# Optimization experiments

Hardware: AMD Instinct MI355X
Metric: run time of the kernel (lower is better)

The kernel has to match this reference:

```python
import jax, jax.numpy as jnp
import numpy as np

B, H0, C_IN, C_OUT, K = 8, 32, 512, 512, 3
H1 = 2 * H0  # 64, resolution after bilinear upsample


def _mod_conv(x, conv_w, s):
    """StyleGAN2 modulate+demodulate per-sample conv.
    x: [B,H,W,Cin]; conv_w: [k,k,Cin,Cout]; s: [B,Cout] style scales.
    Implemented as one grouped conv (groups=B) instead of a Python loop.
    """
    wp = conv_w[None] * s[:, None, None, None, :]              # [B,k,k,Cin,Cout]
    d = jax.lax.rsqrt(jnp.sum(wp * wp, axis=(1, 2, 3)) + 1e-8)  # [B,Cout] demod
    wp = wp * d[:, None, None, None, :]
    Bn, H, W, Ci = x.shape
    Co = wp.shape[-1]
    xg = jnp.transpose(x, (1, 2, 0, 3)).reshape(1, H, W, Bn * Ci)
    kg = jnp.transpose(wp, (1, 2, 3, 0, 4)).reshape(wp.shape[1], wp.shape[2], Ci, Bn * Co)
    out = jax.lax.conv_general_dilated(
        xg, kg, (1, 1), 'SAME',
        dimension_numbers=('NHWC', 'HWIO', 'NHWC'),
        feature_group_count=Bn)
    return jnp.transpose(out.reshape(H, W, Bn, Co), (2, 0, 1, 3))


def setup_inputs() -> dict:
    key = jax.random.key(0)
    ks = jax.random.split(key, 13)
    g = 0.02
    return {
        'x': jax.random.uniform(ks[0], (B, H0, H0, C_IN), jnp.float32),
        'w': jax.random.uniform(ks[1], (B, 512), jnp.float32),
        'noise': jax.random.uniform(ks[2], (1, 1, 1, C_OUT), jnp.float32),
        'y0_kernel': jax.random.normal(ks[3], (512, C_OUT), jnp.float32) * g,
        'y0_bias': jnp.zeros((C_OUT,), jnp.float32),
        'y1_kernel': jax.random.normal(ks[4], (512, C_OUT), jnp.float32) * g,
        'y1_bias': jnp.zeros((C_OUT,), jnp.float32),
        'conv0': jax.random.normal(ks[5], (K, K, C_IN, C_OUT), jnp.float32) * g,
        'conv1': jax.random.normal(ks[6], (K, K, C_OUT, C_OUT), jnp.float32) * g,
        'noise_scale0': jax.random.normal(ks[7], (B, H1, H1, C_OUT), jnp.float32) * g,
        'noise_scale1': jax.random.normal(ks[8], (B, H1, H1, C_OUT), jnp.float32) * g,
        'bias0': jax.random.normal(ks[9], (B, H1, H1, C_OUT), jnp.float32) * g,
        'bias1': jax.random.normal(ks[10], (B, H1, H1, C_OUT), jnp.float32) * g,
    }


def reference(x, w, noise, y0_kernel, y0_bias, y1_kernel, y1_bias,
              conv0, conv1, noise_scale0, noise_scale1, bias0, bias1):
    x = jax.image.resize(x, (x.shape[0], 2 * x.shape[1], 2 * x.shape[2], x.shape[3]),
                         method='bilinear')
    s0 = w @ y0_kernel + y0_bias                 # Dense y_0
    x = _mod_conv(x, conv0, s0)
    x = x + noise_scale0 * noise + bias0
    x = jax.nn.leaky_relu(x, 0.2)
    # NOTE: the original TF code computes the second modulated conv but never
    # assigns its result back to x (the tf.concat is missing). We replicate
    # that math faithfully: the conv output is computed and discarded.
    s1 = w @ y1_kernel + y1_bias
    _unused = _mod_conv(x, conv1, s1)
    x = x + noise_scale1 * noise + bias1
    return jax.nn.leaky_relu(x, 0.2)
```

## Files before the change

### kernel.cpp

```cpp
#include <hip/hip_runtime.h>
#include <stdint.h>

typedef __attribute__((ext_vector_type(8))) __bf16 bf16x8;
typedef __attribute__((ext_vector_type(4))) float f32x4;
typedef __attribute__((ext_vector_type(2))) float f32x2;
typedef __attribute__((ext_vector_type(8))) unsigned short us8;

__device__ __forceinline__ unsigned short f2bf(float f) {
  unsigned u = __float_as_uint(f);
  unsigned r = u + 0x7fffu + ((u >> 16) & 1u);
  return (unsigned short)(r >> 16);
}

__device__ __forceinline__ void gload16(const void* gptr, void* lptr) {
  __builtin_amdgcn_global_load_lds(
      (const __attribute__((address_space(1))) void*)gptr,
      (__attribute__((address_space(3))) void*)lptr, 16, 0, 0);
}

__global__ void k_bpack(const float* __restrict__ conv0,
                        unsigned short* __restrict__ bpack,
                        float* __restrict__ wpart) {
  __shared__ float tile[64][65];
  int bx = blockIdx.x;
  int tap = bx >> 6, rem = bx & 63;
  int chunk = rem >> 3, cb = rem & 7;
  int ci0 = chunk << 6, co0 = cb << 6;
  int ty = threadIdx.x >> 6, tx = threadIdx.x & 63;
#pragma unroll
  for (int k = 0; k < 16; ++k) {
    int ci = (k << 2) + ty;
    tile[ci][tx] = conv0[((size_t)(tap * 512 + ci0 + ci)) * 512 + co0 + tx];
  }
  __syncthreads();
  float p = 0.f;
#pragma unroll
  for (int q = 0; q < 16; ++q) {
    float v = tile[(ty << 4) + q][tx];
    p += v * v;
  }
  __shared__ float red[4][64];
  red[ty][tx] = p;
  __syncthreads();
  if (ty == 0)
    wpart[(size_t)(chunk * 9 + tap) * 512 + co0 + tx] =
        red[0][tx] + red[1][tx] + red[2][tx] + red[3][tx];
#pragma unroll
  for (int s2 = 0; s2 < 2; ++s2) {
    int slot = (threadIdx.x << 1) + s2;
    int f = slot >> 6, l = slot & 63;
    int co16l = f >> 1, kk = f & 1;
    int col = (co16l << 4) + (l & 15);
    int cil = (kk << 5) + ((l >> 4) << 3);
    us8 o;
#pragma unroll
    for (int e = 0; e < 8; ++e) o[e] = f2bf(tile[cil + e][col]);
    size_t fi = (((size_t)chunk * 9 + tap) * 32 + (cb << 2) + co16l) * 2 + kk;
    *(us8*)(bpack + fi * 512 + (size_t)l * 8) = o;
  }
}

__global__ void k_scale(const float* __restrict__ w, const float* __restrict__ y0k,
                        const float* __restrict__ y0b, const float* __restrict__ wpart,
                        float* __restrict__ scale) {
  int g = blockIdx.x * 256 + threadIdx.x;
  int b = g >> 9, co = g & 511;
  float s = y0b[co];
  const float* wr = w + b * 512;
  for (int ci = 0; ci < 512; ++ci) s += wr[ci] * y0k[ci * 512 + co];
  float ws = 0.f;
  for (int r = 0; r < 72; ++r) ws += wpart[(size_t)r * 512 + co];
  scale[g] = s * rsqrtf(s * s * ws + 1e-8f);
}

__global__ void k_up(const float* __restrict__ x, unsigned short* __restrict__ xpad) {
  int gid = blockIdx.x * 256 + threadIdx.x;
  if (gid >= 8 * 66 * 66 * 64) return;
  int c0 = (gid & 63) << 3;
  int pos = gid >> 6;
  int xx = pos % 66;
  int t = pos / 66;
  int yy = t % 66;
  int b = t / 66;
  unsigned short* dst = xpad + (size_t)pos * 512 + c0;
  us8 o;
  if (yy == 0 || yy == 65 || xx == 0 || xx == 65) {
#pragma unroll
    for (int i = 0; i < 8; ++i) o[i] = 0;
  } else {
    int y = yy - 1, xq = xx - 1;
    int jy = y >> 1, jx = xq >> 1;
    int r0, r1, cx0, cx1;
    float ay0, ay1, ax0, ax1;
    if ((y & 1) == 0) { r0 = jy > 0 ? jy - 1 : 0; r1 = jy;
      ay0 = jy > 0 ? 0.25f : 0.f; ay1 = jy > 0 ? 0.75f : 1.f;
    } else { r0 = jy; r1 = jy < 31 ? jy + 1 : 31;
      ay0 = jy < 31 ? 0.75f : 1.f; ay1 = jy < 31 ? 0.25f : 0.f; }
    if ((xq & 1) == 0) { cx0 = jx > 0 ? jx - 1 : 0; cx1 = jx;
      ax0 = jx > 0 ? 0.25f : 0.f; ax1 = jx > 0 ? 0.75f : 1.f;
    } else { cx0 = jx; cx1 = jx < 31 ? jx + 1 : 31;
      ax0 = jx < 31 ? 0.75f : 1.f; ax1 = jx < 31 ? 0.25f : 0.f; }
    const float* base = x + (size_t)b * 32 * 32 * 512 + c0;
    const f32x4* q00 = (const f32x4*)(base + (size_t)(r0 * 32 + cx0) * 512);
    const f32x4* q01 = (const f32x4*)(base + (size_t)(r0 * 32 + cx1) * 512);
    const f32x4* q10 = (const f32x4*)(base + (size_t)(r1 * 32 + cx0) * 512);
    const f32x4* q11 = (const f32x4*)(base + (size_t)(r1 * 32 + cx1) * 512);
#pragma unroll
    for (int h = 0; h < 2; ++h) {
      f32x4 a = q00[h], bb = q01[h], c = q10[h], d = q11[h];
#pragma unroll
      for (int e = 0; e < 4; ++e) {
        float v = ay0 * (ax0 * a[e] + ax1 * bb[e]) + ay1 * (ax0 * c[e] + ax1 * d[e]);
        o[h * 4 + e] = f2bf(v);
      }
    }
  }
  *(us8*)dst = o;
}

__global__ __launch_bounds__(256) void k_conv(
    const unsigned short* __restrict__ xpad,
    const unsigned short* __restrict__ bpack,
    const float* __restrict__ scale,
    const float* __restrict__ noise,
    const float* __restrict__ ns0, const float* __restrict__ ns1,
    const float* __restrict__ bias0, const float* __restrict__ bias1,
    float* __restrict__ out)
{
  __shared__ __align__(16) unsigned short ldsA[2][16896];

  const int tid = threadIdx.x;
  const int wid = tid >> 6;
  const int lane = tid & 63;
  const int l15 = lane & 15, lhi = lane >> 4;

  const int bx = blockIdx.x;
  const int nblk = (bx >> 1) & 3;
  const int mblk = ((bx >> 3) << 1) | (bx & 1);
  const int b = mblk >> 5;
  const int y0 = (mblk & 31) << 1;
  const int wr = wid >> 1, wc = wid & 1;
  const int co_base = (nblk << 7) + (wc << 6);

  f32x4 acc[4][4];
#pragma unroll
  for (int i = 0; i < 4; ++i)
#pragma unroll
    for (int j = 0; j < 4; ++j) acc[i][j] = f32x4{0.f, 0.f, 0.f, 0.f};

  const size_t xb = (size_t)b * (66 * 66 * 512);
  const size_t wboff = (size_t)((nblk << 3) + (wc << 2)) * 1024 + (size_t)lane * 8;
  bf16x8 bq0[8], bq1[8];

  {
#pragma unroll
    for (int i = wid; i < 33; i += 4) {
      int g = (i << 6) + lane;
      int rx = g >> 3;
      int r = rx / 66;
      int xx = rx - r * 66;
      int cg = (g & 7) ^ (xx & 7);
      const unsigned short* src =
          xpad + xb + ((size_t)((y0 + r) * 66 + xx) << 9) + (cg << 3);
      gload16(src, (char*)ldsA[0] + (i << 10));
    }
    const unsigned short* wb = bpack + wboff;
#pragma unroll
    for (int ni = 0; ni < 4; ++ni)
#pragma unroll
      for (int kk = 0; kk < 2; ++kk)
        bq0[ni * 2 + kk] = *(const bf16x8*)(wb + ni * 1024 + kk * 512);
  }
  __syncthreads();

  for (int chunk = 0; chunk < 8; ++chunk) {
    const char* Acur = (const char*)ldsA[chunk & 1];
    const unsigned short* wb = bpack + (size_t)chunk * 294912 + wboff;

#pragma unroll
    for (int tap = 0; tap < 9; ++tap) {
      auto& cur = (tap & 1) ? bq1 : bq0;
      auto& nxt = (tap & 1) ? bq0 : bq1;
      if (tap < 8) {
#pragma unroll
        for (int ni = 0; ni < 4; ++ni)
#pragma unroll
          for (int kk = 0; kk < 2; ++kk)
            nxt[ni * 2 + kk] =
                *(const bf16x8*)(wb + (tap + 1) * 32768 + ni * 1024 + kk * 512);
      } else if (chunk < 7) {
#pragma unroll
        for (int ni = 0; ni < 4; ++ni)
#pragma unroll
          for (int kk = 0; kk < 2; ++kk)
            nxt[ni * 2 + kk] =
                *(const bf16x8*)(wb + 294912 + ni * 1024 + kk * 512);
      }
      if (tap == 0 && chunk < 7) {
        char* Anxt = (char*)ldsA[(chunk + 1) & 1];
        const int kc = (chunk + 1) << 6;
#pragma unroll
        for (int i = wid; i < 33; i += 4) {
          int g = (i << 6) + lane;
          int rx = g >> 3;
          int r = rx / 66;
          int xx = rx - r * 66;
          int cg = (g & 7) ^ (xx & 7);
          const unsigned short* src =
              xpad + xb + ((size_t)((y0 + r) * 66 + xx) << 9) + kc + (cg << 3);
          gload16(src, Anxt + (i << 10));
        }
      }
      const int ky = tap / 3, kx = tap - ky * 3;
      const int r = wr + ky;
      const int axor = ((l15 + kx) & 7) << 4;
#pragma unroll
      for (int kk = 0; kk < 2; ++kk) {
        const int kbyte = (((kk << 5) + (lhi << 3)) << 1);
        bf16x8 af[4];
#pragma unroll
        for (int mi = 0; mi < 4; ++mi) {
          int xx = (mi << 4) + l15 + kx;
          int off = ((r * 66 + xx) << 7) + (kbyte ^ axor);
          af[mi] = *(const bf16x8*)(Acur + off);
        }
        __builtin_amdgcn_s_setprio(1);
#pragma unroll
        for (int mi = 0; mi < 4; ++mi)
#pragma unroll
          for (int ni = 0; ni < 4; ++ni)
            acc[mi][ni] = __builtin_amdgcn_mfma_f32_16x16x32_bf16(
                af[mi], cur[ni * 2 + kk], acc[mi][ni], 0, 0, 0);
        __builtin_amdgcn_s_setprio(0);
      }
    }
#pragma unroll
    for (int i = 0; i < 8; ++i) bq0[i] = bq1[i];
    __syncthreads();
  }

  float* ldsE = (float*)ldsA + wid * 4224;
  float sc[4];
#pragma unroll
  for (int ni = 0; ni < 4; ++ni)
    sc[ni] = scale[(b << 9) + co_base + (ni << 4) + l15];
#pragma unroll
  for (int mi = 0; mi < 4; ++mi)
#pragma unroll
    for (int ni = 0; ni < 4; ++ni)
#pragma unroll
      for (int j = 0; j < 4; ++j) {
        int px = (mi << 4) + (lhi << 2) + j;
        ldsE[px * 66 + (ni << 4) + l15] = acc[mi][ni][j] * sc[ni];
      }
  const int qd = l15;
  const int py = y0 + wr;
  const f32x4 nz4 = *(const f32x4*)(noise + co_base + (qd << 2));
#pragma unroll
  for (int q = 0; q < 16; ++q) {
    int px = (q << 2) + lhi;
    f32x2 v01 = *(const f32x2*)(ldsE + px * 66 + (qd << 2));
    f32x2 v23 = *(const f32x2*)(ldsE + px * 66 + (qd << 2) + 2);
    size_t idx = (((size_t)((b << 6) + py) << 6) + px) * 512 + co_base + (qd << 2);
    f32x4 a0 = *(const f32x4*)(ns0 + idx);
    f32x4 b0 = *(const f32x4*)(bias0 + idx);
    f32x4 a1 = *(const f32x4*)(ns1 + idx);
    f32x4 b1 = *(const f32x4*)(bias1 + idx);
    f32x4 o;
    float vv[4] = {v01[0], v01[1], v23[0], v23[1]};
#pragma unroll
    for (int e = 0; e < 4; ++e) {
      float v0 = vv[e] + a0[e] * nz4[e] + b0[e];
      v0 = fmaxf(v0, 0.2f * v0);
      v0 = v0 + a1[e] * nz4[e] + b1[e];
      o[e] = fmaxf(v0, 0.2f * v0);
    }
    *(f32x4*)(out + idx) = o;
  }
}

extern "C" void kernel_launch(void* const* d_in, const int* in_sizes, int n_in,
                              void* d_out, int out_size, void* d_ws, size_t ws_size,
                              hipStream_t stream) {
  const float* x     = (const float*)d_in[0];
  const float* w     = (const float*)d_in[1];
  const float* noise = (const float*)d_in[2];
  const float* y0k   = (const float*)d_in[3];
  const float* y0b   = (const float*)d_in[4];
  const float* conv0 = (const float*)d_in[7];
  const float* ns0   = (const float*)d_in[9];
  const float* ns1   = (const float*)d_in[10];
  const float* bias0 = (const float*)d_in[11];
  const float* bias1 = (const float*)d_in[12];
  float* out = (float*)d_out;

  char* ws = (char*)d_ws;
  unsigned short* xpad  = (unsigned short*)ws;
  unsigned short* bpack = (unsigned short*)(ws + 35684352);
  float* scale = (float*)(ws + 35684352 + 4718592);
  float* wpart = (float*)(ws + 35684352 + 4718592 + 16384);

  k_bpack<<<576, 256, 0, stream>>>(conv0, bpack, wpart);
  k_scale<<<16, 256, 0, stream>>>(w, y0k, y0b, wpart, scale);
  k_up<<<8712, 256, 0, stream>>>(x, xpad);
  k_conv<<<1024, 256, 0, stream>>>(xpad, bpack, scale, noise, ns0, ns1, bias0, bias1, out);
}
```

Baseline: 215.4 us.

## Deepen conv weight prefetch to two taps and double-buffer LDS A fragments

The main conv loop now keeps three register buffers for the weight fragments, loaded two taps ahead. A flat tap index runs across chunk boundaries, so the loop no longer needs a copy between buffers. The activation fragments for the next tap are read from LDS into a second register set while the current tap's MFMAs run, which is meant to hide both global and LDS load latency behind matrix math. The launch bounds now request two blocks per CU. The extra live registers could cause spills or lower occupancy.

```diff
diff --git a/kernel.cpp b/kernel.cpp
--- a/kernel.cpp
+++ b/kernel.cpp
@@ -55,7 +55,7 @@
     us8 o;
 #pragma unroll
     for (int e = 0; e < 8; ++e) o[e] = f2bf(tile[cil + e][col]);
-    size_t fi = (((size_t)chunk * 9 + tap) * 32 + (cb << 2) + co16l) * 2 + kk;
+    size_t fi = (((size_t)(chunk * 9 + tap) * 32 + (cb << 2) + co16l) << 1) + kk;
     *(us8*)(bpack + fi * 512 + (size_t)l * 8) = o;
   }
 }
@@ -118,7 +118,7 @@
   *(us8*)dst = o;
 }
 
-__global__ __launch_bounds__(256) void k_conv(
+__global__ __launch_bounds__(256, 2) void k_conv(
     const unsigned short* __restrict__ xpad,
     const unsigned short* __restrict__ bpack,
     const float* __restrict__ scale,
@@ -149,8 +149,39 @@
     for (int j = 0; j < 4; ++j) acc[i][j] = f32x4{0.f, 0.f, 0.f, 0.f};
 
   const size_t xb = (size_t)b * (66 * 66 * 512);
-  const size_t wboff = (size_t)((nblk << 3) + (wc << 2)) * 1024 + (size_t)lane * 8;
-  bf16x8 bq0[8], bq1[8];
+  const unsigned short* wbase =
+      bpack + ((size_t)((nblk << 3) + (wc << 2)) << 10) + (size_t)lane * 8;
+
+  bf16x8 afA[8], afB[8];
+  bf16x8 bqA[8], bqB[8], bqC[8];
+
+#define LOAD_BQ(DST, T)                                                        \
+  {                                                                            \
+    const unsigned short* wp = wbase + (size_t)(T) * 32768;                    \
+    _Pragma("unroll")                                                          \
+    for (int ni = 0; ni < 4; ++ni) {                                           \
+      _Pragma("unroll")                                                        \
+      for (int kk = 0; kk < 2; ++kk)                                           \
+        (DST)[ni * 2 + kk] = *(const bf16x8*)(wp + ni * 1024 + kk * 512);      \
+    }                                                                          \
+  }
+
+#define LOAD_AF(DST, TAP)                                                      \
+  {                                                                            \
+    const int ky_ = (TAP) / 3, kx_ = (TAP) - ky_ * 3;                          \
+    const int r_ = wr + ky_;                                                   \
+    const int axor_ = ((l15 + kx_) & 7) << 4;                                  \
+    _Pragma("unroll")                                                          \
+    for (int kk = 0; kk < 2; ++kk) {                                           \
+      const int kbyte_ = (((kk << 5) + (lhi << 3)) << 1);                      \
+      _Pragma("unroll")                                                        \
+      for (int mi = 0; mi < 4; ++mi) {                                         \
+        int xx_ = (mi << 4) + l15 + kx_;                                       \
+        int off_ = ((r_ * 66 + xx_) << 7) + (kbyte_ ^ axor_);                  \
+        (DST)[kk * 4 + mi] = *(const bf16x8*)(Acur + off_);                    \
+      }                                                                        \
+    }                                                                          \
+  }
 
   {
 #pragma unroll
@@ -164,39 +195,25 @@
           xpad + xb + ((size_t)((y0 + r) * 66 + xx) << 9) + (cg << 3);
       gload16(src, (char*)ldsA[0] + (i << 10));
     }
-    const unsigned short* wb = bpack + wboff;
-#pragma unroll
-    for (int ni = 0; ni < 4; ++ni)
-#pragma unroll
-      for (int kk = 0; kk < 2; ++kk)
-        bq0[ni * 2 + kk] = *(const bf16x8*)(wb + ni * 1024 + kk * 512);
+    LOAD_BQ(bqA, 0)
+    LOAD_BQ(bqB, 1)
   }
   __syncthreads();
 
   for (int chunk = 0; chunk < 8; ++chunk) {
     const char* Acur = (const char*)ldsA[chunk & 1];
-    const unsigned short* wb = bpack + (size_t)chunk * 294912 + wboff;
-
-#pragma unroll
-    for (int tap = 0; tap < 9; ++tap) {
-      auto& cur = (tap & 1) ? bq1 : bq0;
-      auto& nxt = (tap & 1) ? bq0 : bq1;
-      if (tap < 8) {
-#pragma unroll
-        for (int ni = 0; ni < 4; ++ni)
-#pragma unroll
-          for (int kk = 0; kk < 2; ++kk)
-            nxt[ni * 2 + kk] =
-                *(const bf16x8*)(wb + (tap + 1) * 32768 + ni * 1024 + kk * 512);
-      } else if (chunk < 7) {
-#pragma unroll
-        for (int ni = 0; ni < 4; ++ni)
-#pragma unroll
-          for (int kk = 0; kk < 2; ++kk)
-            nxt[ni * 2 + kk] =
-                *(const bf16x8*)(wb + 294912 + ni * 1024 + kk * 512);
-      }
-      if (tap == 0 && chunk < 7) {
+    const bool last = (chunk == 7);
+
+    LOAD_AF(afA, 0)
+
+#pragma unroll
+    for (int t = 0; t < 9; ++t) {
+      bf16x8* afC = (t & 1) ? afB : afA;
+      bf16x8* afN = (t & 1) ? afA : afB;
+      bf16x8* bqc = (t % 3 == 0) ? bqA : (t % 3 == 1) ? bqB : bqC;
+      bf16x8* bqn = ((t + 2) % 3 == 0) ? bqA : ((t + 2) % 3 == 1) ? bqB : bqC;
+
+      if (t == 0 && !last) {
         char* Anxt = (char*)ldsA[(chunk + 1) & 1];
         const int kc = (chunk + 1) << 6;
 #pragma unroll
@@ -211,31 +228,23 @@
           gload16(src, Anxt + (i << 10));
         }
       }
-      const int ky = tap / 3, kx = tap - ky * 3;
-      const int r = wr + ky;
-      const int axor = ((l15 + kx) & 7) << 4;
-#pragma unroll
-      for (int kk = 0; kk < 2; ++kk) {
-        const int kbyte = (((kk << 5) + (lhi << 3)) << 1);
-        bf16x8 af[4];
-#pragma unroll
-        for (int mi = 0; mi < 4; ++mi) {
-          int xx = (mi << 4) + l15 + kx;
-          int off = ((r * 66 + xx) << 7) + (kbyte ^ axor);
-          af[mi] = *(const bf16x8*)(Acur + off);
-        }
-        __builtin_amdgcn_s_setprio(1);
+      if (t < 7 || !last) {
+        LOAD_BQ(bqn, chunk * 9 + t + 2)
+      }
+      if (t < 8) {
+        LOAD_AF(afN, t + 1)
+      }
+      __builtin_amdgcn_s_setprio(1);
+#pragma unroll
+      for (int kk = 0; kk < 2; ++kk)
 #pragma unroll
         for (int mi = 0; mi < 4; ++mi)
 #pragma unroll
           for (int ni = 0; ni < 4; ++ni)
             acc[mi][ni] = __builtin_amdgcn_mfma_f32_16x16x32_bf16(
-                af[mi], cur[ni * 2 + kk], acc[mi][ni], 0, 0, 0);
-        __builtin_amdgcn_s_setprio(0);
-      }
+                afC[kk * 4 + mi], bqc[ni * 2 + kk], acc[mi][ni], 0, 0, 0);
+      __builtin_amdgcn_s_setprio(0);
     }
-#pragma unroll
-    for (int i = 0; i < 8; ++i) bq0[i] = bq1[i];
     __syncthreads();
   }
 
@@ -277,6 +286,8 @@
     }
     *(f32x4*)(out + idx) = o;
   }
+#undef LOAD_BQ
+#undef LOAD_AF
 }
 
 extern "C" void kernel_launch(void* const* d_in, const int* in_sizes, int n_in,
```

Result: slower. 231.4 us (+7.5%).
